# Performance work log

Measured on AMD Instinct MI355X. Metric: run time of the kernel, lower is better.

Reference implementation:

```python
import jax, jax.numpy as jnp
import numpy as np

B, DIM, H, W = 64, 512, 16, 20
HID = DIM // 2          # 256, MutualAttention hidden
HEADS = 8
NZ, NX = 64, 256        # template (8x8) and search (16x16) token counts
EPS_NORM = 1e-12
EPS_LN = 1e-5


def setup_inputs() -> dict:
    key = jax.random.key(0)
    ks = jax.random.split(key, 16)
    s = 0.02
    return {
        "x1": jax.random.normal(ks[0], (B, DIM, H, W), jnp.float32),
        "x2": jax.random.normal(ks[1], (B, DIM, H, W), jnp.float32),
        "W_lin": jax.random.normal(ks[2], (DIM, 2 * DIM), jnp.float32) * s,
        "b_lin": jnp.zeros((2 * DIM,), jnp.float32),
        "W_down": jax.random.normal(ks[3], (DIM, HID), jnp.float32) * s,
        "b_down": jnp.zeros((HID,), jnp.float32),
        "W_up": jax.random.normal(ks[4], (HID, DIM), jnp.float32) * s,
        "b_up": jnp.zeros((DIM,), jnp.float32),
        "Wq": jax.random.normal(ks[5], (HID, HID), jnp.float32) * s,
        "Wk": jax.random.normal(ks[6], (HID, HID), jnp.float32) * s,
        "Wv": jax.random.normal(ks[7], (HID, HID), jnp.float32) * s,
        "Wo": jax.random.normal(ks[8], (HID, HID), jnp.float32) * s,
        "temperature": jnp.ones((HEADS, 1, 1), jnp.float32),
        "W_end": jax.random.normal(ks[9], (DIM, DIM), jnp.float32) * s,
        "b_end": jnp.zeros((DIM,), jnp.float32),
        "gamma": jnp.ones((DIM,), jnp.float32),
        "beta": jnp.zeros((DIM,), jnp.float32),
    }


def _l2norm(x):
    n = jnp.sqrt(jnp.sum(x * x, axis=-1, keepdims=True))
    return x / jnp.maximum(n, EPS_NORM)


def _branch(zx, zy, W_down, b_down, W_up, b_up, Wq, Wk, Wv, Wo, temperature):
    # zx, zy: [B, n, DIM] tokens; conv1x1 == per-token linear so spatial reshape is a no-op
    res = zx
    a = jax.nn.relu(zx @ W_down + b_down)   # [B, n, HID]  (k, v source)
    b_ = jax.nn.relu(zy @ W_down + b_down)  # [B, n, HID]  (q source)
    xb = jnp.swapaxes(a, 1, 2)              # [B, HID, n]
    yb = jnp.swapaxes(b_, 1, 2)
    res1 = xb
    q = jnp.einsum('oc,bcn->bon', Wq, yb)
    k = jnp.einsum('oc,bcn->bon', Wk, xb)
    v = jnp.einsum('oc,bcn->bon', Wv, xb)
    bsz, _, n = q.shape
    c = HID // HEADS
    q = _l2norm(q.reshape(bsz, HEADS, c, n))
    k = _l2norm(k.reshape(bsz, HEADS, c, n))
    v = v.reshape(bsz, HEADS, c, n)
    attn = jnp.einsum('bhcn,bhdn->bhcd', q, k) * temperature  # [B, H, c, c]
    attn = jax.nn.softmax(attn, axis=-1)
    out = jnp.einsum('bhcd,bhdn->bhcn', attn, v).reshape(bsz, HID, n)
    out = jnp.einsum('oc,bcn->bon', Wo, out)
    out = res1 + out                          # [B, HID, n]
    tok = jnp.swapaxes(out, 1, 2)             # [B, n, HID]
    return res + tok @ W_up + b_up            # [B, n, DIM]


def reference(x1, x2, W_lin, b_lin, W_down, b_down, W_up, b_up,
              Wq, Wk, Wv, Wo, temperature, W_end, b_end, gamma, beta):
    bsz = x1.shape[0]
    t1 = jnp.swapaxes(x1.reshape(bsz, DIM, H * W), 1, 2)  # [B, N, DIM]
    t2 = jnp.swapaxes(x2.reshape(bsz, DIM, H * W), 1, 2)
    h1 = jax.nn.relu(t1 @ W_lin + b_lin)
    h2 = jax.nn.relu(t2 @ W_lin + b_lin)
    y1, u1 = h1[..., :DIM], h1[..., DIM:]
    y2, u2 = h2[..., :DIM], h2[..., DIM:]
    # MutualAttention: template tokens (first 64) and search tokens (rest)
    o_z = _branch(u1[:, :NZ], u2[:, :NZ], W_down, b_down, W_up, b_up, Wq, Wk, Wv, Wo, temperature)
    o_x = _branch(u1[:, NZ:], u2[:, NZ:], W_down, b_down, W_up, b_up, Wq, Wk, Wv, Wo, temperature)
    v1 = jnp.concatenate([o_z, o_x], axis=1)  # [B, N, DIM]
    y = y1 + v1
    pre = t1 + (y @ W_end + b_end)
    mu = jnp.mean(pre, axis=-1, keepdims=True)
    var = jnp.mean((pre - mu) ** 2, axis=-1, keepdims=True)
    ln = (pre - mu) / jnp.sqrt(var + EPS_LN) * gamma + beta
    return jnp.swapaxes(ln, 1, 2).reshape(bsz, DIM, H, W)
```

## Files before the change

### kernel.cpp

```cpp
#include <hip/hip_runtime.h>
#include <math.h>

#define NTOK 320
#define BB   64
#define RTOT (BB * NTOK)
#define DIMC 512
#define HIDC 256
#define NHEAD 8

typedef unsigned short u16;
typedef __attribute__((ext_vector_type(8))) short bf8_t;
typedef __attribute__((ext_vector_type(4))) float f4_t;
typedef __attribute__((ext_vector_type(4))) unsigned short us4_t;
typedef __attribute__((ext_vector_type(4))) unsigned int  u4_t;

#define F_BIAS  1
#define F_RELU  2
#define F_F32   4
#define F_PACK  8
#define F_RES1P 16
#define F_RES2P 32
#define F_RESX1 64

__device__ __forceinline__ void bsplit(float f, u16& h, u16& l) {
    const unsigned u = __float_as_uint(f);
    h = (u16)(u >> 16);
    const float fl = f - __uint_as_float(u & 0xffff0000u);
    l = (u16)(__float_as_uint(fl) >> 16);
}
__device__ __forceinline__ float brecon(u16 h, u16 l) {
    return __uint_as_float((unsigned)h << 16) + __uint_as_float((unsigned)l << 16);
}

__global__ __launch_bounds__(256)
void pack_w_k(const float* __restrict__ Wlin, const float* __restrict__ Wdown,
              const float* __restrict__ Wup,  const float* __restrict__ Wend,
              const float* __restrict__ Wq,   const float* __restrict__ Wk,
              const float* __restrict__ Wv,   const float* __restrict__ Wo,
              u16* __restrict__ Ph, u16* __restrict__ Pl)
{
    const int idx = blockIdx.x * 256 + threadIdx.x;
    if (idx >= 1310720) return;
    float v;
    int i = idx;
    if      (i < 524288) { const int j = i >> 9, d = i & 511; v = Wlin[d * 1024 + j]; }
    else if (i < 655360) { i -= 524288; const int j = i >> 9, d = i & 511; v = Wdown[d * 256 + j]; }
    else if (i < 786432) { i -= 655360; const int j = i >> 8, d = i & 255; v = Wup[d * 512 + j]; }
    else if (i < 1048576){ i -= 786432; const int j = i >> 9, d = i & 511; v = Wend[d * 512 + j]; }
    else if (i < 1114112){ v = Wq[i - 1048576]; }
    else if (i < 1245184){ i -= 1114112; v = (i < 65536) ? Wk[i] : Wv[i - 65536]; }
    else                 { v = Wo[i - 1245184]; }
    u16 h, l; bsplit(v, h, l);
    Ph[idx] = h; Pl[idx] = l;
}

__global__ __launch_bounds__(256)
void pack_x_k(const float* __restrict__ x1, const float* __restrict__ x2,
              u16* __restrict__ X1h, u16* __restrict__ X1l,
              u16* __restrict__ X2h, u16* __restrict__ X2l)
{
    __shared__ float tile[64 * 65];
    const int b = blockIdx.z & 63, which = blockIdx.z >> 6;
    const float* src = which ? x2 : x1;
    u16* Dh = which ? X2h : X1h;
    u16* Dl = which ? X2l : X1l;
    const int c0 = blockIdx.x << 6, n0 = blockIdx.y << 6;
    const int t = threadIdx.x, col = t & 63, rq = t >> 6;
    const float* sb_ = src + (long)b * DIMC * NTOK;
    #pragma unroll
    for (int i = 0; i < 16; ++i) {
        const int c = rq * 16 + i;
        tile[c * 65 + col] = sb_[(long)(c0 + c) * NTOK + n0 + col];
    }
    __syncthreads();
    #pragma unroll
    for (int i = 0; i < 16; ++i) {
        const int nr = rq * 16 + i;
        u16 h, l; bsplit(tile[col * 65 + nr], h, l);
        const long o = (long)(b * NTOK + n0 + nr) * DIMC + c0 + col;
        Dh[o] = h; Dl[o] = l;
    }
}

template<int FLAGS>
__global__ __launch_bounds__(256)
void gemm_tm(const u16* __restrict__ Agh, const u16* __restrict__ Agl,
             const u16* __restrict__ Bgh, const u16* __restrict__ Bgl,
             int Dk,
             float* __restrict__ Cf, int ldcf,
             u16* __restrict__ Ch, u16* __restrict__ Cl, int ldcp,
             const float* __restrict__ bias,
             const u16* __restrict__ R1h, const u16* __restrict__ R1l, int ldr1,
             const u16* __restrict__ R2h, const u16* __restrict__ R2l, int ldr2,
             const float* __restrict__ xres)
{
    __shared__ __align__(16) u16 Ah[128 * 40], Al[128 * 40];
    __shared__ __align__(16) u16 Bh[64 * 40],  Bl[64 * 40];

    const int j0 = blockIdx.x * 128;
    const int r0 = blockIdx.y * 64;
    const int t = threadIdx.x, lane = t & 63, wave = t >> 6;
    const int wm = wave >> 1, wn = wave & 1;
    const int r16 = lane & 15, g = lane >> 4;

    f4_t acc[4][2];
    #pragma unroll
    for (int i = 0; i < 4; ++i)
        #pragma unroll
        for (int j = 0; j < 2; ++j)
            acc[i][j] = (f4_t){0.f, 0.f, 0.f, 0.f};

    for (int d0 = 0; d0 < Dk; d0 += 32) {
        {
            const int row0 = t >> 2,        c0_ = (t & 3) << 3;
            const int row1 = (t >> 2) + 64;
            const long a0 = (long)(j0 + row0) * Dk + d0 + c0_;
            const long a1 = (long)(j0 + row1) * Dk + d0 + c0_;
            *(u4_t*)&Ah[row0 * 40 + c0_] = *(const u4_t*)&Agh[a0];
            *(u4_t*)&Ah[row1 * 40 + c0_] = *(const u4_t*)&Agh[a1];
            *(u4_t*)&Al[row0 * 40 + c0_] = *(const u4_t*)&Agl[a0];
            *(u4_t*)&Al[row1 * 40 + c0_] = *(const u4_t*)&Agl[a1];
            const long ab = (long)(r0 + row0) * Dk + d0 + c0_;
            *(u4_t*)&Bh[row0 * 40 + c0_] = *(const u4_t*)&Bgh[ab];
            *(u4_t*)&Bl[row0 * 40 + c0_] = *(const u4_t*)&Bgl[ab];
        }
        __syncthreads();

        bf8_t ah[4], al[4], bh[2], bl[2];
        #pragma unroll
        for (int fm = 0; fm < 4; ++fm) {
            const int m = wm * 64 + fm * 16 + r16;
            ah[fm] = *(const bf8_t*)&Ah[m * 40 + g * 8];
            al[fm] = *(const bf8_t*)&Al[m * 40 + g * 8];
        }
        #pragma unroll
        for (int fn = 0; fn < 2; ++fn) {
            const int rr = wn * 32 + fn * 16 + r16;
            bh[fn] = *(const bf8_t*)&Bh[rr * 40 + g * 8];
            bl[fn] = *(const bf8_t*)&Bl[rr * 40 + g * 8];
        }
        #pragma unroll
        for (int fm = 0; fm < 4; ++fm)
            #pragma unroll
            for (int fn = 0; fn < 2; ++fn) {
                acc[fm][fn] = __builtin_amdgcn_mfma_f32_16x16x32_bf16(ah[fm], bh[fn], acc[fm][fn], 0, 0, 0);
                acc[fm][fn] = __builtin_amdgcn_mfma_f32_16x16x32_bf16(ah[fm], bl[fn], acc[fm][fn], 0, 0, 0);
                acc[fm][fn] = __builtin_amdgcn_mfma_f32_16x16x32_bf16(al[fm], bh[fn], acc[fm][fn], 0, 0, 0);
            }
        __syncthreads();
    }

    const int bb = r0 / NTOK, nn0 = r0 % NTOK;
    #pragma unroll
    for (int fm = 0; fm < 4; ++fm) {
        const int jb = j0 + wm * 64 + fm * 16 + g * 4;
        f4_t bv = (f4_t){0.f, 0.f, 0.f, 0.f};
        if (FLAGS & F_BIAS) bv = *(const f4_t*)&bias[jb];
        #pragma unroll
        for (int fn = 0; fn < 2; ++fn) {
            const int r = r0 + wn * 32 + fn * 16 + r16;
            f4_t v = acc[fm][fn];
            if (FLAGS & F_BIAS) v += bv;
            if (FLAGS & F_RES1P) {
                const us4_t rh = *(const us4_t*)&R1h[(long)r * ldr1 + jb];
                const us4_t rl = *(const us4_t*)&R1l[(long)r * ldr1 + jb];
                #pragma unroll
                for (int q = 0; q < 4; ++q) v[q] += brecon(rh[q], rl[q]);
            }
            if (FLAGS & F_RES2P) {
                const us4_t rh = *(const us4_t*)&R2h[(long)r * ldr2 + jb];
                const us4_t rl = *(const us4_t*)&R2l[(long)r * ldr2 + jb];
                #pragma unroll
                for (int q = 0; q < 4; ++q) v[q] += brecon(rh[q], rl[q]);
            }
            if (FLAGS & F_RESX1) {
                const int nl = nn0 + wn * 32 + fn * 16 + r16;
                #pragma unroll
                for (int q = 0; q < 4; ++q)
                    v[q] += xres[(long)bb * DIMC * NTOK + (long)(jb + q) * NTOK + nl];
            }
            if (FLAGS & F_RELU) {
                #pragma unroll
                for (int q = 0; q < 4; ++q) v[q] = fmaxf(v[q], 0.f);
            }
            if (FLAGS & F_F32)
                *(f4_t*)&Cf[(long)r * ldcf + jb] = v;
            if (FLAGS & F_PACK) {
                us4_t h4, l4;
                #pragma unroll
                for (int q = 0; q < 4; ++q) { u16 h, l; bsplit(v[q], h, l); h4[q] = h; l4[q] = l; }
                *(us4_t*)&Ch[(long)r * ldcp + jb] = h4;
                *(us4_t*)&Cl[(long)r * ldcp + jb] = l4;
            }
        }
    }
}

__global__ __launch_bounds__(256)
void attn_tm(const float* __restrict__ Qf, const float* __restrict__ KVf,
             u16* __restrict__ AOh, u16* __restrict__ AOl,
             const float* __restrict__ temp)
{
    const int slice = blockIdx.x, h = blockIdx.y, b = blockIdx.z;
    const int rb = b * NTOK + (slice ? 64 : 0);
    const int Nt = slice ? 256 : 64;
    const int qc = h * 32;

    __shared__ float ks[256 * 33], vs[256 * 33];
    __shared__ float PT[32 * 36];
    __shared__ float invq[32], invk[32];
    const int t = threadIdx.x;

    for (int q = t; q < Nt * 8; q += 256) {
        const int n = q >> 3, c4 = (q & 7) << 2;
        *(f4_t*)&ks[n * 33 + c4] = *(const f4_t*)&KVf[(long)(rb + n) * 512 + qc + c4];
        *(f4_t*)&vs[n * 33 + c4] = *(const f4_t*)&KVf[(long)(rb + n) * 512 + 256 + qc + c4];
    }
    __syncthreads();

    {
        const int c = t >> 3, l8 = t & 7;
        float sq = 0.f, sk = 0.f;
        for (int n = l8; n < Nt; n += 8) {
            const float qv = Qf[(long)(rb + n) * 256 + qc + c];
            sq = fmaf(qv, qv, sq);
            const float kv = ks[n * 33 + c];
            sk = fmaf(kv, kv, sk);
        }
        sq += __shfl_xor(sq, 1); sq += __shfl_xor(sq, 2); sq += __shfl_xor(sq, 4);
        sk += __shfl_xor(sk, 1); sk += __shfl_xor(sk, 2); sk += __shfl_xor(sk, 4);
        if (l8 == 0) {
            invq[c] = 1.f / fmaxf(sqrtf(sq), 1e-12f);
            invk[c] = 1.f / fmaxf(sqrtf(sk), 1e-12f);
        }
    }
    __syncthreads();

    {
        const int c = t >> 3, db = (t & 7) << 2;
        float s0 = 0.f, s1 = 0.f, s2 = 0.f, s3 = 0.f;
        for (int n = 0; n < Nt; n += 4) {
            #pragma unroll
            for (int u = 0; u < 4; ++u) {
                const float qv = Qf[(long)(rb + n + u) * 256 + qc + c];
                const int o = (n + u) * 33 + db;
                s0 = fmaf(qv, ks[o + 0], s0);
                s1 = fmaf(qv, ks[o + 1], s1);
                s2 = fmaf(qv, ks[o + 2], s2);
                s3 = fmaf(qv, ks[o + 3], s3);
            }
        }
        const float sc = invq[c] * temp[h];
        const float l0 = s0 * sc * invk[db + 0];
        const float l1 = s1 * sc * invk[db + 1];
        const float l2 = s2 * sc * invk[db + 2];
        const float l3 = s3 * sc * invk[db + 3];
        float m = fmaxf(fmaxf(l0, l1), fmaxf(l2, l3));
        m = fmaxf(m, __shfl_xor(m, 1));
        m = fmaxf(m, __shfl_xor(m, 2));
        m = fmaxf(m, __shfl_xor(m, 4));
        const float e0 = expf(l0 - m), e1 = expf(l1 - m);
        const float e2 = expf(l2 - m), e3 = expf(l3 - m);
        float s = e0 + e1 + e2 + e3;
        s += __shfl_xor(s, 1); s += __shfl_xor(s, 2); s += __shfl_xor(s, 4);
        const float inv = 1.f / s;
        PT[(db + 0) * 36 + c] = e0 * inv;
        PT[(db + 1) * 36 + c] = e1 * inv;
        PT[(db + 2) * 36 + c] = e2 * inv;
        PT[(db + 3) * 36 + c] = e3 * inv;
    }
    __syncthreads();

    for (int idx = t; idx < Nt * 8; idx += 256) {
        const int n = idx >> 3, cq = (idx & 7) << 2;
        f4_t o = (f4_t){0.f, 0.f, 0.f, 0.f};
        #pragma unroll 8
        for (int d = 0; d < 32; ++d) {
            const float vv = vs[n * 33 + d];
            const f4_t p = *(const f4_t*)&PT[d * 36 + cq];
            o += p * vv;
        }
        us4_t h4, l4;
        #pragma unroll
        for (int q = 0; q < 4; ++q) { u16 h, l; bsplit(o[q], h, l); h4[q] = h; l4[q] = l; }
        const long oadr = (long)(rb + n) * 256 + qc + cq;
        *(us4_t*)&AOh[oadr] = h4;
        *(us4_t*)&AOl[oadr] = l4;
    }
}

__global__ __launch_bounds__(256)
void ln_tm(const float* __restrict__ PREf, const float* __restrict__ gamma,
           const float* __restrict__ beta, float* __restrict__ out)
{
    __shared__ float tile[64 * 65];
    __shared__ float sb[64 * 4], s2b[64 * 4];
    __shared__ float muS[64], rsS[64];
    const int r0 = blockIdx.x << 6;
    const int b = r0 / NTOK, n0 = r0 % NTOK;
    const int t = threadIdx.x;
    {
        const int tok = t >> 2, qq = t & 3;
        const float* row = PREf + (long)(r0 + tok) * 512 + qq * 128;
        float s = 0.f, s2 = 0.f;
        #pragma unroll 8
        for (int i = 0; i < 32; ++i) {
            const f4_t v4 = *(const f4_t*)&row[i * 4];
            s += v4[0] + v4[1] + v4[2] + v4[3];
            s2 = fmaf(v4[0], v4[0], s2); s2 = fmaf(v4[1], v4[1], s2);
            s2 = fmaf(v4[2], v4[2], s2); s2 = fmaf(v4[3], v4[3], s2);
        }
        sb[tok * 4 + qq] = s; s2b[tok * 4 + qq] = s2;
    }
    __syncthreads();
    if (t < 64) {
        const float s  = sb[t * 4] + sb[t * 4 + 1] + sb[t * 4 + 2] + sb[t * 4 + 3];
        const float s2 = s2b[t * 4] + s2b[t * 4 + 1] + s2b[t * 4 + 2] + s2b[t * 4 + 3];
        const float mu = s * (1.f / 512.f);
        const float var = s2 * (1.f / 512.f) - mu * mu;
        muS[t] = mu;
        rsS[t] = 1.f / sqrtf(var + 1e-5f);
    }
    __syncthreads();
    const int cc = t & 63, tq = t >> 6;
    for (int ct = 0; ct < 8; ++ct) {
        const float ga = gamma[ct * 64 + cc], be = beta[ct * 64 + cc];
        #pragma unroll
        for (int i = 0; i < 16; ++i) {
            const int tok = tq * 16 + i;
            const float v = PREf[(long)(r0 + tok) * 512 + ct * 64 + cc];
            tile[cc * 65 + tok] = (v - muS[tok]) * rsS[tok] * ga + be;
        }
        __syncthreads();
        #pragma unroll
        for (int i = 0; i < 16; ++i) {
            const int ccr = tq * 16 + i;
            out[(long)b * DIMC * NTOK + (long)(ct * 64 + ccr) * NTOK + n0 + cc] = tile[ccr * 65 + cc];
        }
        __syncthreads();
    }
}

extern "C" void kernel_launch(void* const* d_in, const int* in_sizes, int n_in,
                              void* d_out, int out_size, void* d_ws, size_t ws_size,
                              hipStream_t stream)
{
    const float* x1     = (const float*)d_in[0];
    const float* x2     = (const float*)d_in[1];
    const float* W_lin  = (const float*)d_in[2];
    const float* b_lin  = (const float*)d_in[3];
    const float* W_down = (const float*)d_in[4];
    const float* b_down = (const float*)d_in[5];
    const float* W_up   = (const float*)d_in[6];
    const float* b_up   = (const float*)d_in[7];
    const float* Wq     = (const float*)d_in[8];
    const float* Wk     = (const float*)d_in[9];
    const float* Wv     = (const float*)d_in[10];
    const float* Wo     = (const float*)d_in[11];
    const float* temp   = (const float*)d_in[12];
    const float* W_end  = (const float*)d_in[13];
    const float* b_end  = (const float*)d_in[14];
    const float* gamma  = (const float*)d_in[15];
    const float* beta   = (const float*)d_in[16];

    const size_t MB = 1ull << 20;
    char* base = (char*)d_ws;
    u16* X1h = (u16*)(base + 0 * MB);
    u16* X1l = (u16*)(base + 20 * MB);
    u16* X2h = (u16*)(base + 40 * MB);
    u16* X2l = (u16*)(base + 60 * MB);
    u16* Wph = (u16*)(base + 80 * MB);
    u16* Wpl = (u16*)(base + 80 * MB + 2621440);
    u16* Y1h = (u16*)(base + 85 * MB);
    u16* Y1l = (u16*)(base + 105 * MB);
    u16* U1h = (u16*)(base + 125 * MB);
    u16* U1l = (u16*)(base + 145 * MB);
    u16* U2h = (u16*)(base + 165 * MB);
    u16* U2l = (u16*)(base + 185 * MB);
    u16* XBh = (u16*)(base + 205 * MB);
    u16* XBl = (u16*)(base + 215 * MB);
    float* Qf  = (float*)(base + 0 * MB);
    u16* AOh   = (u16*)(base + 20 * MB);
    u16* AOl   = (u16*)(base + 30 * MB);
    u16* OCh   = (u16*)(base + 0 * MB);
    u16* OCl   = (u16*)(base + 10 * MB);
    u16* YBh   = (u16*)(base + 40 * MB);
    u16* YBl   = (u16*)(base + 50 * MB);
    float* KVf = (float*)(base + 40 * MB);
    float* PREf= (float*)(base + 40 * MB);
    u16* Yh    = (u16*)(base + 165 * MB);
    u16* Yl    = (u16*)(base + 185 * MB);

    const long WL = 0, WD = 524288, WU = 655360, WE = 786432,
               WQ = 1048576, WKV = 1114112, WO = 1245184;

    const dim3 blk(256);

    pack_x_k<<<dim3(8, 5, 128), blk, 0, stream>>>(x1, x2, X1h, X1l, X2h, X2l);
    pack_w_k<<<dim3(5120), blk, 0, stream>>>(W_lin, W_down, W_up, W_end, Wq, Wk, Wv, Wo, Wph, Wpl);

    gemm_tm<F_BIAS | F_RELU | F_PACK><<<dim3(4, 320), blk, 0, stream>>>(
        Wph + WL, Wpl + WL, X1h, X1l, 512,
        nullptr, 0, Y1h, Y1l, 512, b_lin,
        nullptr, nullptr, 0, nullptr, nullptr, 0, nullptr);
    gemm_tm<F_BIAS | F_RELU | F_PACK><<<dim3(4, 320), blk, 0, stream>>>(
        Wph + WL + 512 * 512, Wpl + WL + 512 * 512, X1h, X1l, 512,
        nullptr, 0, U1h, U1l, 512, b_lin + 512,
        nullptr, nullptr, 0, nullptr, nullptr, 0, nullptr);
    gemm_tm<F_BIAS | F_RELU | F_PACK><<<dim3(4, 320), blk, 0, stream>>>(
        Wph + WL + 512 * 512, Wpl + WL + 512 * 512, X2h, X2l, 512,
        nullptr, 0, U2h, U2l, 512, b_lin + 512,
        nullptr, nullptr, 0, nullptr, nullptr, 0, nullptr);
    gemm_tm<F_BIAS | F_RELU | F_PACK><<<dim3(2, 320), blk, 0, stream>>>(
        Wph + WD, Wpl + WD, U1h, U1l, 512,
        nullptr, 0, XBh, XBl, 256, b_down,
        nullptr, nullptr, 0, nullptr, nullptr, 0, nullptr);
    gemm_tm<F_BIAS | F_RELU | F_PACK><<<dim3(2, 320), blk, 0, stream>>>(
        Wph + WD, Wpl + WD, U2h, U2l, 512,
        nullptr, 0, YBh, YBl, 256, b_down,
        nullptr, nullptr, 0, nullptr, nullptr, 0, nullptr);
    gemm_tm<F_F32><<<dim3(2, 320), blk, 0, stream>>>(
        Wph + WQ, Wpl + WQ, YBh, YBl, 256,
        Qf, 256, nullptr, nullptr, 0, nullptr,
        nullptr, nullptr, 0, nullptr, nullptr, 0, nullptr);
    gemm_tm<F_F32><<<dim3(4, 320), blk, 0, stream>>>(
        Wph + WKV, Wpl + WKV, XBh, XBl, 256,
        KVf, 512, nullptr, nullptr, 0, nullptr,
        nullptr, nullptr, 0, nullptr, nullptr, 0, nullptr);
    attn_tm<<<dim3(2, NHEAD, BB), blk, 0, stream>>>(Qf, KVf, AOh, AOl, temp);
    gemm_tm<F_PACK | F_RES1P><<<dim3(2, 320), blk, 0, stream>>>(
        Wph + WO, Wpl + WO, AOh, AOl, 256,
        nullptr, 0, OCh, OCl, 256, nullptr,
        XBh, XBl, 256, nullptr, nullptr, 0, nullptr);
    gemm_tm<F_BIAS | F_PACK | F_RES1P | F_RES2P><<<dim3(4, 320), blk, 0, stream>>>(
        Wph + WU, Wpl + WU, OCh, OCl, 256,
        nullptr, 0, Yh, Yl, 512, b_up,
        Y1h, Y1l, 512, U1h, U1l, 512, nullptr);
    gemm_tm<F_BIAS | F_F32 | F_RESX1><<<dim3(4, 320), blk, 0, stream>>>(
        Wph + WE, Wpl + WE, Yh, Yl, 512,
        PREf, 512, nullptr, nullptr, 0, b_end,
        nullptr, nullptr, 0, nullptr, nullptr, 0, x1);
    ln_tm<<<dim3(320), blk, 0, stream>>>(PREf, gamma, beta, (float*)d_out);
}
```

Before: 669.1 us.

## Load GEMM fragments directly from global with 128x128 tiles and XCD-aware block remap

The GEMM kernel drops LDS staging and its barriers: each wave loads its bf16 hi/lo MFMA fragments straight from global memory. The output tile grows from 128x64 to 128x128, giving 4x4 accumulators per wave. Blocks are launched on a 1D grid and remapped so neighbouring tiles land on the same XCD for L2 reuse, and K depth becomes a template constant. The attention kernel now stages Q in LDS instead of V and reads V rows directly from global. The cost is uncoalesced 16-byte global fragment loads that depend on L2 hits, plus higher register pressure.

```diff
diff --git a/kernel.cpp b/kernel.cpp
--- a/kernel.cpp
+++ b/kernel.cpp
@@ -12,7 +12,6 @@
 typedef __attribute__((ext_vector_type(8))) short bf8_t;
 typedef __attribute__((ext_vector_type(4))) float f4_t;
 typedef __attribute__((ext_vector_type(4))) unsigned short us4_t;
-typedef __attribute__((ext_vector_type(4))) unsigned int  u4_t;
 
 #define F_BIAS  1
 #define F_RELU  2
@@ -82,11 +81,10 @@
     }
 }
 
-template<int FLAGS>
+template<int FLAGS, int DK, int JB>
 __global__ __launch_bounds__(256)
 void gemm_tm(const u16* __restrict__ Agh, const u16* __restrict__ Agl,
              const u16* __restrict__ Bgh, const u16* __restrict__ Bgl,
-             int Dk,
              float* __restrict__ Cf, int ldcf,
              u16* __restrict__ Ch, u16* __restrict__ Cl, int ldcp,
              const float* __restrict__ bias,
@@ -94,71 +92,56 @@
              const u16* __restrict__ R2h, const u16* __restrict__ R2l, int ldr2,
              const float* __restrict__ xres)
 {
-    __shared__ __align__(16) u16 Ah[128 * 40], Al[128 * 40];
-    __shared__ __align__(16) u16 Bh[64 * 40],  Bl[64 * 40];
-
-    const int j0 = blockIdx.x * 128;
-    const int r0 = blockIdx.y * 64;
+    const int nwg = JB * 160;
+    const int nb  = (blockIdx.x & 7) * (nwg >> 3) + (blockIdx.x >> 3);
+    const int j0 = (nb % JB) * 128;
+    const int r0 = (nb / JB) * 128;
+
     const int t = threadIdx.x, lane = t & 63, wave = t >> 6;
-    const int wm = wave >> 1, wn = wave & 1;
+    const int wq = wave >> 1, wr = wave & 1;
     const int r16 = lane & 15, g = lane >> 4;
 
-    f4_t acc[4][2];
+    const int aoff = (j0 + wq * 64 + r16) * DK + g * 8;
+    const int boff = (r0 + wr * 64 + r16) * DK + g * 8;
+
+    f4_t acc[4][4];
     #pragma unroll
     for (int i = 0; i < 4; ++i)
         #pragma unroll
-        for (int j = 0; j < 2; ++j)
+        for (int j = 0; j < 4; ++j)
             acc[i][j] = (f4_t){0.f, 0.f, 0.f, 0.f};
 
-    for (int d0 = 0; d0 < Dk; d0 += 32) {
-        {
-            const int row0 = t >> 2,        c0_ = (t & 3) << 3;
-            const int row1 = (t >> 2) + 64;
-            const long a0 = (long)(j0 + row0) * Dk + d0 + c0_;
-            const long a1 = (long)(j0 + row1) * Dk + d0 + c0_;
-            *(u4_t*)&Ah[row0 * 40 + c0_] = *(const u4_t*)&Agh[a0];
-            *(u4_t*)&Ah[row1 * 40 + c0_] = *(const u4_t*)&Agh[a1];
-            *(u4_t*)&Al[row0 * 40 + c0_] = *(const u4_t*)&Agl[a0];
-            *(u4_t*)&Al[row1 * 40 + c0_] = *(const u4_t*)&Agl[a1];
-            const long ab = (long)(r0 + row0) * Dk + d0 + c0_;
-            *(u4_t*)&Bh[row0 * 40 + c0_] = *(const u4_t*)&Bgh[ab];
-            *(u4_t*)&Bl[row0 * 40 + c0_] = *(const u4_t*)&Bgl[ab];
-        }
-        __syncthreads();
-
-        bf8_t ah[4], al[4], bh[2], bl[2];
+    #pragma unroll 2
+    for (int d0 = 0; d0 < DK; d0 += 32) {
+        bf8_t ah[4], al[4], bh[4], bl[4];
         #pragma unroll
         for (int fm = 0; fm < 4; ++fm) {
-            const int m = wm * 64 + fm * 16 + r16;
-            ah[fm] = *(const bf8_t*)&Ah[m * 40 + g * 8];
-            al[fm] = *(const bf8_t*)&Al[m * 40 + g * 8];
-        }
-        #pragma unroll
-        for (int fn = 0; fn < 2; ++fn) {
-            const int rr = wn * 32 + fn * 16 + r16;
-            bh[fn] = *(const bf8_t*)&Bh[rr * 40 + g * 8];
-            bl[fn] = *(const bf8_t*)&Bl[rr * 40 + g * 8];
+            ah[fm] = *(const bf8_t*)&Agh[aoff + fm * 16 * DK + d0];
+            al[fm] = *(const bf8_t*)&Agl[aoff + fm * 16 * DK + d0];
+        }
+        #pragma unroll
+        for (int fn = 0; fn < 4; ++fn) {
+            bh[fn] = *(const bf8_t*)&Bgh[boff + fn * 16 * DK + d0];
+            bl[fn] = *(const bf8_t*)&Bgl[boff + fn * 16 * DK + d0];
         }
         #pragma unroll
         for (int fm = 0; fm < 4; ++fm)
             #pragma unroll
-            for (int fn = 0; fn < 2; ++fn) {
+            for (int fn = 0; fn < 4; ++fn) {
                 acc[fm][fn] = __builtin_amdgcn_mfma_f32_16x16x32_bf16(ah[fm], bh[fn], acc[fm][fn], 0, 0, 0);
                 acc[fm][fn] = __builtin_amdgcn_mfma_f32_16x16x32_bf16(ah[fm], bl[fn], acc[fm][fn], 0, 0, 0);
                 acc[fm][fn] = __builtin_amdgcn_mfma_f32_16x16x32_bf16(al[fm], bh[fn], acc[fm][fn], 0, 0, 0);
             }
-        __syncthreads();
-    }
-
-    const int bb = r0 / NTOK, nn0 = r0 % NTOK;
+    }
+
     #pragma unroll
     for (int fm = 0; fm < 4; ++fm) {
-        const int jb = j0 + wm * 64 + fm * 16 + g * 4;
+        const int jb = j0 + wq * 64 + fm * 16 + g * 4;
         f4_t bv = (f4_t){0.f, 0.f, 0.f, 0.f};
         if (FLAGS & F_BIAS) bv = *(const f4_t*)&bias[jb];
         #pragma unroll
-        for (int fn = 0; fn < 2; ++fn) {
-            const int r = r0 + wn * 32 + fn * 16 + r16;
+        for (int fn = 0; fn < 4; ++fn) {
+            const int r = r0 + wr * 64 + fn * 16 + r16;
             f4_t v = acc[fm][fn];
             if (FLAGS & F_BIAS) v += bv;
             if (FLAGS & F_RES1P) {
@@ -174,10 +157,12 @@
                 for (int q = 0; q < 4; ++q) v[q] += brecon(rh[q], rl[q]);
             }
             if (FLAGS & F_RESX1) {
-                const int nl = nn0 + wn * 32 + fn * 16 + r16;
+                const unsigned rr = (unsigned)r;
+                const int bb = rr / 320u;
+                const int nn = rr - bb * 320u;
                 #pragma unroll
                 for (int q = 0; q < 4; ++q)
-                    v[q] += xres[(long)bb * DIMC * NTOK + (long)(jb + q) * NTOK + nl];
+                    v[q] += xres[(long)bb * DIMC * NTOK + (long)(jb + q) * NTOK + nn];
             }
             if (FLAGS & F_RELU) {
                 #pragma unroll
@@ -206,15 +191,15 @@
     const int Nt = slice ? 256 : 64;
     const int qc = h * 32;
 
-    __shared__ float ks[256 * 33], vs[256 * 33];
+    __shared__ float qs[256 * 34], ks[256 * 34];
     __shared__ float PT[32 * 36];
     __shared__ float invq[32], invk[32];
     const int t = threadIdx.x;
 
     for (int q = t; q < Nt * 8; q += 256) {
         const int n = q >> 3, c4 = (q & 7) << 2;
-        *(f4_t*)&ks[n * 33 + c4] = *(const f4_t*)&KVf[(long)(rb + n) * 512 + qc + c4];
-        *(f4_t*)&vs[n * 33 + c4] = *(const f4_t*)&KVf[(long)(rb + n) * 512 + 256 + qc + c4];
+        *(f4_t*)&qs[n * 34 + c4] = *(const f4_t*)&Qf[(long)(rb + n) * 256 + qc + c4];
+        *(f4_t*)&ks[n * 34 + c4] = *(const f4_t*)&KVf[(long)(rb + n) * 512 + qc + c4];
     }
     __syncthreads();
 
@@ -222,9 +207,9 @@
         const int c = t >> 3, l8 = t & 7;
         float sq = 0.f, sk = 0.f;
         for (int n = l8; n < Nt; n += 8) {
-            const float qv = Qf[(long)(rb + n) * 256 + qc + c];
+            const float qv = qs[n * 34 + c];
             sq = fmaf(qv, qv, sq);
-            const float kv = ks[n * 33 + c];
+            const float kv = ks[n * 34 + c];
             sk = fmaf(kv, kv, sk);
         }
         sq += __shfl_xor(sq, 1); sq += __shfl_xor(sq, 2); sq += __shfl_xor(sq, 4);
@@ -239,16 +224,13 @@
     {
         const int c = t >> 3, db = (t & 7) << 2;
         float s0 = 0.f, s1 = 0.f, s2 = 0.f, s3 = 0.f;
-        for (int n = 0; n < Nt; n += 4) {
-            #pragma unroll
-            for (int u = 0; u < 4; ++u) {
-                const float qv = Qf[(long)(rb + n + u) * 256 + qc + c];
-                const int o = (n + u) * 33 + db;
-                s0 = fmaf(qv, ks[o + 0], s0);
-                s1 = fmaf(qv, ks[o + 1], s1);
-                s2 = fmaf(qv, ks[o + 2], s2);
-                s3 = fmaf(qv, ks[o + 3], s3);
-            }
+        for (int n = 0; n < Nt; ++n) {
+            const float qv = qs[n * 34 + c];
+            const int o = n * 34 + db;
+            s0 = fmaf(qv, ks[o + 0], s0);
+            s1 = fmaf(qv, ks[o + 1], s1);
+            s2 = fmaf(qv, ks[o + 2], s2);
+            s3 = fmaf(qv, ks[o + 3], s3);
         }
         const float sc = invq[c] * temp[h];
         const float l0 = s0 * sc * invk[db + 0];
@@ -273,12 +255,14 @@
 
     for (int idx = t; idx < Nt * 8; idx += 256) {
         const int n = idx >> 3, cq = (idx & 7) << 2;
+        const float* Vrow = &KVf[(long)(rb + n) * 512 + 256 + qc];
         f4_t o = (f4_t){0.f, 0.f, 0.f, 0.f};
-        #pragma unroll 8
-        for (int d = 0; d < 32; ++d) {
-            const float vv = vs[n * 33 + d];
-            const f4_t p = *(const f4_t*)&PT[d * 36 + cq];
-            o += p * vv;
+        #pragma unroll
+        for (int d4 = 0; d4 < 8; ++d4) {
+            const f4_t vv = *(const f4_t*)&Vrow[d4 * 4];
+            #pragma unroll
+            for (int u = 0; u < 4; ++u)
+                o += *(const f4_t*)&PT[(d4 * 4 + u) * 36 + cq] * vv[u];
         }
         us4_t h4, l4;
         #pragma unroll
@@ -399,45 +383,45 @@
     pack_x_k<<<dim3(8, 5, 128), blk, 0, stream>>>(x1, x2, X1h, X1l, X2h, X2l);
     pack_w_k<<<dim3(5120), blk, 0, stream>>>(W_lin, W_down, W_up, W_end, Wq, Wk, Wv, Wo, Wph, Wpl);
 
-    gemm_tm<F_BIAS | F_RELU | F_PACK><<<dim3(4, 320), blk, 0, stream>>>(
-        Wph + WL, Wpl + WL, X1h, X1l, 512,
+    gemm_tm<F_BIAS | F_RELU | F_PACK, 512, 4><<<dim3(640), blk, 0, stream>>>(
+        Wph + WL, Wpl + WL, X1h, X1l,
         nullptr, 0, Y1h, Y1l, 512, b_lin,
         nullptr, nullptr, 0, nullptr, nullptr, 0, nullptr);
-    gemm_tm<F_BIAS | F_RELU | F_PACK><<<dim3(4, 320), blk, 0, stream>>>(
-        Wph + WL + 512 * 512, Wpl + WL + 512 * 512, X1h, X1l, 512,
+    gemm_tm<F_BIAS | F_RELU | F_PACK, 512, 4><<<dim3(640), blk, 0, stream>>>(
+        Wph + WL + 512 * 512, Wpl + WL + 512 * 512, X1h, X1l,
         nullptr, 0, U1h, U1l, 512, b_lin + 512,
         nullptr, nullptr, 0, nullptr, nullptr, 0, nullptr);
-    gemm_tm<F_BIAS | F_RELU | F_PACK><<<dim3(4, 320), blk, 0, stream>>>(
-        Wph + WL + 512 * 512, Wpl + WL + 512 * 512, X2h, X2l, 512,
+    gemm_tm<F_BIAS | F_RELU | F_PACK, 512, 4><<<dim3(640), blk, 0, stream>>>(
+        Wph + WL + 512 * 512, Wpl + WL + 512 * 512, X2h, X2l,
         nullptr, 0, U2h, U2l, 512, b_lin + 512,
         nullptr, nullptr, 0, nullptr, nullptr, 0, nullptr);
-    gemm_tm<F_BIAS | F_RELU | F_PACK><<<dim3(2, 320), blk, 0, stream>>>(
-        Wph + WD, Wpl + WD, U1h, U1l, 512,
+    gemm_tm<F_BIAS | F_RELU | F_PACK, 512, 2><<<dim3(320), blk, 0, stream>>>(
+        Wph + WD, Wpl + WD, U1h, U1l,
         nullptr, 0, XBh, XBl, 256, b_down,
         nullptr, nullptr, 0, nullptr, nullptr, 0, nullptr);
-    gemm_tm<F_BIAS | F_RELU | F_PACK><<<dim3(2, 320), blk, 0, stream>>>(
-        Wph + WD, Wpl + WD, U2h, U2l, 512,
+    gemm_tm<F_BIAS | F_RELU | F_PACK, 512, 2><<<dim3(320), blk, 0, stream>>>(
+        Wph + WD, Wpl + WD, U2h, U2l,
         nullptr, 0, YBh, YBl, 256, b_down,
         nullptr, nullptr, 0, nullptr, nullptr, 0, nullptr);
-    gemm_tm<F_F32><<<dim3(2, 320), blk, 0, stream>>>(
-        Wph + WQ, Wpl + WQ, YBh, YBl, 256,
+    gemm_tm<F_F32, 256, 2><<<dim3(320), blk, 0, stream>>>(
+        Wph + WQ, Wpl + WQ, YBh, YBl,
         Qf, 256, nullptr, nullptr, 0, nullptr,
         nullptr, nullptr, 0, nullptr, nullptr, 0, nullptr);
-    gemm_tm<F_F32><<<dim3(4, 320), blk, 0, stream>>>(
-        Wph + WKV, Wpl + WKV, XBh, XBl, 256,
+    gemm_tm<F_F32, 256, 4><<<dim3(640), blk, 0, stream>>>(
+        Wph + WKV, Wpl + WKV, XBh, XBl,
         KVf, 512, nullptr, nullptr, 0, nullptr,
         nullptr, nullptr, 0, nullptr, nullptr, 0, nullptr);
     attn_tm<<<dim3(2, NHEAD, BB), blk, 0, stream>>>(Qf, KVf, AOh, AOl, temp);
-    gemm_tm<F_PACK | F_RES1P><<<dim3(2, 320), blk, 0, stream>>>(
-        Wph + WO, Wpl + WO, AOh, AOl, 256,
+    gemm_tm<F_PACK | F_RES1P, 256, 2><<<dim3(320), blk, 0, stream>>>(
+        Wph + WO, Wpl + WO, AOh, AOl,
         nullptr, 0, OCh, OCl, 256, nullptr,
         XBh, XBl, 256, nullptr, nullptr, 0, nullptr);
-    gemm_tm<F_BIAS | F_PACK | F_RES1P | F_RES2P><<<dim3(4, 320), blk, 0, stream>>>(
-        Wph + WU, Wpl + WU, OCh, OCl, 256,
+    gemm_tm<F_BIAS | F_PACK | F_RES1P | F_RES2P, 256, 4><<<dim3(640), blk, 0, stream>>>(
+        Wph + WU, Wpl + WU, OCh, OCl,
         nullptr, 0, Yh, Yl, 512, b_up,
         Y1h, Y1l, 512, U1h, U1l, 512, nullptr);
-    gemm_tm<F_BIAS | F_F32 | F_RESX1><<<dim3(4, 320), blk, 0, stream>>>(
-        Wph + WE, Wpl + WE, Yh, Yl, 512,
+    gemm_tm<F_BIAS | F_F32 | F_RESX1, 512, 4><<<dim3(640), blk, 0, stream>>>(
+        Wph + WE, Wpl + WE, Yh, Yl,
         PREf, 512, nullptr, nullptr, 0, b_end,
         nullptr, nullptr, 0, nullptr, nullptr, 0, x1);
     ln_tm<<<dim3(320), blk, 0, stream>>>(PREf, gamma, beta, (float*)d_out);
```

Result: slower. 959.7 us (+43.4%).
